# Kernel optimization log

Hardware: AMD Instinct MI355X
Metric: run time of the kernel (lower is better)

## Reference

```python
import jax, jax.numpy as jnp
import numpy as np

DIM = 1024
NH = 16
HD = DIM // NH  # 64
NT = max(1, int(NH * 0.25))  # 4 time heads
NS = NH - NT                 # 12 space heads
SCALE = HD ** (-0.5)


def setup_inputs() -> dict:
    key = jax.random.key(0)
    ks = jax.random.split(key, 8)
    B, T = 2, 2048
    init = 0.02
    return {
        "x": jax.random.normal(ks[0], (B, T, DIM), dtype=jnp.float32),
        # weights stored as (in, out); torch Linear y = x @ W.T is equivalent
        "Wqt": jax.random.normal(ks[1], (DIM, NT * HD), dtype=jnp.float32) * init,
        "Wkt": jax.random.normal(ks[2], (DIM, NT * HD), dtype=jnp.float32) * init,
        "Wqs": jax.random.normal(ks[3], (DIM, NS * HD), dtype=jnp.float32) * init,
        "Wks": jax.random.normal(ks[4], (DIM, NS * HD), dtype=jnp.float32) * init,
        "Wv": jax.random.normal(ks[5], (DIM, DIM), dtype=jnp.float32) * init,
        "Wout": jax.random.normal(ks[6], (DIM, DIM), dtype=jnp.float32) * init,
        "bout": jnp.zeros((DIM,), dtype=jnp.float32),
        "w_sigma": jnp.zeros((1,), dtype=jnp.float32),
    }


def reference(x, Wqt, Wkt, Wqs, Wks, Wv, Wout, bout, w_sigma):
    B, T, D = x.shape
    Qt = (x @ Wqt).reshape(B, T, NT, HD)
    Kt = (x @ Wkt).reshape(B, T, NT, HD)
    Qs = (x @ Wqs).reshape(B, T, NS, HD)
    Ks = (x @ Wks).reshape(B, T, NS, HD)
    st = jnp.einsum('bthd,bshd->bths', Qt, Kt)  # [B,T,NT,T]
    ss = jnp.einsum('bthd,bshd->bths', Qs, Ks)  # [B,T,NS,T]
    sig = jax.nn.sigmoid(w_sigma)  # shape (1,), broadcasts
    score = jnp.concatenate([-sig * st, ss], axis=2) * SCALE  # [B,T,NH,T]
    attn = jax.nn.softmax(score, axis=-1)
    V = (x @ Wv).reshape(B, T, NH, HD)
    ctx = jnp.einsum('bths,bshd->bthd', attn, V).reshape(B, T, D)
    return ctx @ Wout + bout
```

## Files before the change

### kernel.cpp

```cpp
#include <hip/hip_runtime.h>
#include <hip/hip_bf16.h>

typedef __bf16 bf16_t;
typedef __bf16 bf16x4 __attribute__((ext_vector_type(4)));
typedef __bf16 bf16x8 __attribute__((ext_vector_type(8)));
typedef float  f32x4  __attribute__((ext_vector_type(4)));

#define DIM     1024
#define NHEAD   16
#define HDIM    64
#define NTIME   4
#define TSEQ    2048
#define NBATCH  2
#define SCALE_F 0.125f
#define LOG2E   1.4426950408889634f

#define GLL(gp, lp) __builtin_amdgcn_global_load_lds( \
    (const __attribute__((address_space(1))) unsigned int*)(const void*)(gp), \
    (__attribute__((address_space(3))) unsigned int*)(void*)(lp), 16, 0, 0)

#define OFF_WQKVT 0UL
#define OFF_WOUTT (OFF_WQKVT + 3072UL*1024UL*2UL)
#define OFF_Q     (OFF_WOUTT + 1024UL*1024UL*2UL)
#define OFF_K     (OFF_Q  + 2UL*16UL*2048UL*64UL*2UL)
#define OFF_VT    (OFF_K  + 2UL*16UL*2048UL*64UL*2UL)
#define OFF_CTX   (OFF_VT + 2UL*16UL*2048UL*64UL*2UL)

__global__ void prep_all(const float* __restrict__ x,
                         const float* __restrict__ Wqt, const float* __restrict__ Wkt,
                         const float* __restrict__ Wqs, const float* __restrict__ Wks,
                         const float* __restrict__ Wv,  const float* __restrict__ Wout,
                         bf16_t* __restrict__ Xb, bf16_t* __restrict__ WqkvT,
                         bf16_t* __restrict__ WoutT) {
    __shared__ float T[64][65];
    const int bid = blockIdx.x;
    if (bid < 2048) {
        int i = bid * 256 + threadIdx.x;
        const float4* s = (const float4*)(x + (size_t)i * 8);
        float4 a = s[0], b2 = s[1];
        bf16x8 v;
        v[0] = (bf16_t)a.x;  v[1] = (bf16_t)a.y;  v[2] = (bf16_t)a.z;  v[3] = (bf16_t)a.w;
        v[4] = (bf16_t)b2.x; v[5] = (bf16_t)b2.y; v[6] = (bf16_t)b2.z; v[7] = (bf16_t)b2.w;
        *(bf16x8*)(Xb + (size_t)i * 8) = v;
        return;
    }
    const int tc = threadIdx.x & 63, tr = threadIdx.x >> 6;
    if (bid < 2816) {
        const int l = bid - 2048;
        const int n0 = (l % 48) * 64;
        const int k0 = (l / 48) * 64;
        const int region = n0 >> 10;
        const int cc = n0 & 1023;
        const int h = cc >> 6;
        const float* src; int ncols, col0;
        if (region == 2) { src = Wv; ncols = 1024; col0 = cc; }
        else if (h < NTIME) { src = (region == 0) ? Wqt : Wkt; ncols = NTIME * HDIM; col0 = h * HDIM; }
        else                { src = (region == 0) ? Wqs : Wks; ncols = (NHEAD - NTIME) * HDIM; col0 = (h - NTIME) * HDIM; }
#pragma unroll
        for (int i = 0; i < 16; ++i) {
            int kl = tr * 16 + i;
            T[kl][tc] = src[(size_t)(k0 + kl) * ncols + col0 + tc];
        }
        __syncthreads();
#pragma unroll
        for (int i = 0; i < 16; ++i) {
            int nl = tr * 16 + i;
            WqkvT[(size_t)(n0 + nl) * 1024 + k0 + tc] = (bf16_t)T[tc][nl];
        }
    } else {
        const int l = bid - 2816;
        const int n0 = (l % 16) * 64;
        const int k0 = (l / 16) * 64;
#pragma unroll
        for (int i = 0; i < 16; ++i) {
            int kl = tr * 16 + i;
            T[kl][tc] = Wout[(size_t)(k0 + kl) * 1024 + n0 + tc];
        }
        __syncthreads();
#pragma unroll
        for (int i = 0; i < 16; ++i) {
            int nl = tr * 16 + i;
            WoutT[(size_t)(n0 + nl) * 1024 + k0 + tc] = (bf16_t)T[tc][nl];
        }
    }
}

template<int MODE, int NB>
__global__ __launch_bounds__(256)
void gemm_bf16(const bf16_t* __restrict__ Ab, const bf16_t* __restrict__ Bt,
               bf16_t* __restrict__ Qb, bf16_t* __restrict__ Kb, bf16_t* __restrict__ Vt,
               float* __restrict__ Cout, const float* __restrict__ bias)
{
    __shared__ __align__(16) bf16_t As[3][128][32];
    __shared__ __align__(16) bf16_t Bs[3][128][32];

    constexpr int NXC = NB / 8;
    const int xcd = blockIdx.x & 7;
    const int r   = blockIdx.x >> 3;
    const int m0 = (r / NXC) * 128;
    const int n0 = (xcd * NXC + r % NXC) * 128;

    const int tid  = threadIdx.x;
    const int lane = tid & 63;
    const int wave = tid >> 6;
    const int wm = (wave >> 1) * 64, wn = (wave & 1) * 64;
    const int g = lane >> 4, lr = lane & 15;

    f32x4 acc[4][4];
#pragma unroll
    for (int i = 0; i < 4; ++i)
#pragma unroll
        for (int j = 0; j < 4; ++j) acc[i][j] = f32x4{0.f, 0.f, 0.f, 0.f};

    auto stage = [&](int k0, int buf) {
#pragma unroll
        for (int c = 0; c < 2; ++c) {
            int idx  = tid + c * 256;
            int row  = idx >> 2;
            int csrc = (idx & 3) ^ ((row >> 1) & 3);
            GLL(Ab + (size_t)(m0 + row) * 1024 + k0 + csrc * 8,
                (char*)&As[buf][0][0] + (c * 256 + wave * 64) * 16);
            GLL(Bt + (size_t)(n0 + row) * 1024 + k0 + csrc * 8,
                (char*)&Bs[buf][0][0] + (c * 256 + wave * 64) * 16);
        }
    };

    stage(0, 0);
    stage(32, 1);

    for (int t = 0; t < 32; ++t) {
        if (t < 31) asm volatile("s_waitcnt vmcnt(4)" ::: "memory");
        else        asm volatile("s_waitcnt vmcnt(0)" ::: "memory");
        __builtin_amdgcn_s_barrier();
        __builtin_amdgcn_sched_barrier(0);
        if (t + 2 < 32) stage((t + 2) * 32, (t + 2) % 3);

        const int buf = t % 3;
        const char* Ac = (const char*)&As[buf][0][0];
        const char* Bc = (const char*)&Bs[buf][0][0];
        bf16x8 afr[4], bfr[4];
#pragma unroll
        for (int f = 0; f < 4; ++f) {
            int ra = wm + f * 16 + lr;
            afr[f] = *(const bf16x8*)(Ac + ra * 64 + ((g ^ ((ra >> 1) & 3)) << 4));
            int rb = wn + f * 16 + lr;
            bfr[f] = *(const bf16x8*)(Bc + rb * 64 + ((g ^ ((rb >> 1) & 3)) << 4));
        }
        __builtin_amdgcn_s_setprio(1);
#pragma unroll
        for (int fm = 0; fm < 4; ++fm)
#pragma unroll
            for (int fn = 0; fn < 4; ++fn)
                acc[fm][fn] = __builtin_amdgcn_mfma_f32_16x16x32_bf16(bfr[fn], afr[fm], acc[fm][fn], 0, 0, 0);
        __builtin_amdgcn_s_setprio(0);
    }

    const int region = n0 >> 10;
#pragma unroll
    for (int fm = 0; fm < 4; ++fm) {
        const int m = m0 + wm + fm * 16 + lr;
        const int b = m >> 11, t = m & 2047;
        const int ts = (t & ~31) | (((t >> 2) & 3) << 3) | (((t >> 4) & 1) << 2) | (t & 3);
#pragma unroll
        for (int fn = 0; fn < 4; ++fn) {
            const int nb = n0 + wn + fn * 16 + g * 4;
            if constexpr (MODE == 1) {
                float4 bb = *(const float4*)(bias + nb);
                float4 v;
                v.x = acc[fm][fn][0] + bb.x;
                v.y = acc[fm][fn][1] + bb.y;
                v.z = acc[fm][fn][2] + bb.z;
                v.w = acc[fm][fn][3] + bb.w;
                *(float4*)(Cout + (size_t)m * DIM + nb) = v;
            } else {
                const int cc = nb & 1023;
                const int h = cc >> 6, d0 = cc & 63;
                const size_t bh = (size_t)(b * NHEAD + h);
                if (region == 2) {
#pragma unroll
                    for (int r2 = 0; r2 < 4; ++r2)
                        Vt[(bh * HDIM + d0 + r2) * TSEQ + ts] = (bf16_t)acc[fm][fn][r2];
                } else {
                    bf16x4 w;
#pragma unroll
                    for (int r2 = 0; r2 < 4; ++r2) w[r2] = (bf16_t)acc[fm][fn][r2];
                    bf16_t* dst = (region == 0) ? Qb : Kb;
                    *(bf16x4*)(dst + (bh * TSEQ + t) * HDIM + d0) = w;
                }
            }
        }
    }
}

__global__ __launch_bounds__(256, 2)
void attn_kernel(const bf16_t* __restrict__ Qb, const bf16_t* __restrict__ Kb,
                 const bf16_t* __restrict__ Vt, bf16_t* __restrict__ ctx,
                 const float* __restrict__ w_sigma)
{
    __shared__ __align__(16) bf16_t Ktile[4][64][64];
    __shared__ __align__(16) bf16_t Vtile[4][64][64];

    const int l    = ((blockIdx.x & 7) << 6) + (blockIdx.x >> 3);
    const int qc   = l & 15;
    const int bh   = l >> 4;
    const int h    = bh & 15;
    const int b    = bh >> 4;
    const int tid  = threadIdx.x;
    const int lane = tid & 63;
    const int wave = tid >> 6;
    const int g = lane >> 4, lr = lane & 15;
    const int q0 = qc * 128 + wave * 32;

    const float sig = 1.f / (1.f + __expf(-w_sigma[0]));
    const float fl2 = ((h < NTIME) ? (-sig * SCALE_F) : SCALE_F) * LOG2E;

    const bf16_t* Qp = Qb + (size_t)bh * TSEQ * HDIM;
    const bf16_t* Kp = Kb + (size_t)bh * TSEQ * HDIM;
    const bf16_t* Vp = Vt + (size_t)bh * HDIM * TSEQ;

    bf16x8 qa0 = *(const bf16x8*)(Qp + (size_t)(q0 + lr) * HDIM + g * 8);
    bf16x8 qa1 = *(const bf16x8*)(Qp + (size_t)(q0 + lr) * HDIM + 32 + g * 8);
    bf16x8 qb0 = *(const bf16x8*)(Qp + (size_t)(q0 + 16 + lr) * HDIM + g * 8);
    bf16x8 qb1 = *(const bf16x8*)(Qp + (size_t)(q0 + 16 + lr) * HDIM + 32 + g * 8);
#pragma unroll
    for (int e = 0; e < 8; ++e) {
        qa0[e] = (bf16_t)((float)qa0[e] * fl2);
        qa1[e] = (bf16_t)((float)qa1[e] * fl2);
        qb0[e] = (bf16_t)((float)qb0[e] * fl2);
        qb1[e] = (bf16_t)((float)qb1[e] * fl2);
    }

    f32x4 oA[4], oB[4];
#pragma unroll
    for (int n = 0; n < 4; ++n) { oA[n] = f32x4{0.f,0.f,0.f,0.f}; oB[n] = f32x4{0.f,0.f,0.f,0.f}; }
    float lpA = 0.f, lpB = 0.f;

    const int trow = tid >> 3;
    const int tcg  = tid & 7;

    auto stage = [&](int s0, int buf) {
#pragma unroll
        for (int j = 0; j < 2; ++j) {
            int kr = j * 32 + trow;
            GLL(Kp + (size_t)(s0 + kr) * HDIM + ((tcg ^ (kr & 7)) << 3),
                (char*)&Ktile[buf][0][0] + (j * 256 + wave * 64) * 16);
            int vr = j * 32 + trow;
            GLL(Vp + (size_t)vr * TSEQ + s0 + ((tcg ^ (vr & 7)) << 3),
                (char*)&Vtile[buf][0][0] + (j * 256 + wave * 64) * 16);
        }
    };

    auto compute = [&](const char* Kt, const char* Vc) {
        bf16x4 wA[4], wB[4];
        __builtin_amdgcn_s_setprio(1);
#pragma unroll
        for (int st = 0; st < 4; ++st) {
            const int srow = st * 16 + lr;
            const int rs7 = lr & 7;
            bf16x8 kb0 = *(const bf16x8*)(Kt + srow * 128 + ((g ^ rs7) << 4));
            bf16x8 kb1 = *(const bf16x8*)(Kt + srow * 128 + (((4 + g) ^ rs7) << 4));
            f32x4 zA = f32x4{0.f,0.f,0.f,0.f}, zB = f32x4{0.f,0.f,0.f,0.f};
            zA = __builtin_amdgcn_mfma_f32_16x16x32_bf16(kb0, qa0, zA, 0, 0, 0);
            zA = __builtin_amdgcn_mfma_f32_16x16x32_bf16(kb1, qa1, zA, 0, 0, 0);
            zB = __builtin_amdgcn_mfma_f32_16x16x32_bf16(kb0, qb0, zB, 0, 0, 0);
            zB = __builtin_amdgcn_mfma_f32_16x16x32_bf16(kb1, qb1, zB, 0, 0, 0);
            float a0 = __builtin_amdgcn_exp2f(zA[0]);
            float a1 = __builtin_amdgcn_exp2f(zA[1]);
            float a2 = __builtin_amdgcn_exp2f(zA[2]);
            float a3 = __builtin_amdgcn_exp2f(zA[3]);
            float b0 = __builtin_amdgcn_exp2f(zB[0]);
            float b1 = __builtin_amdgcn_exp2f(zB[1]);
            float b2 = __builtin_amdgcn_exp2f(zB[2]);
            float b3 = __builtin_amdgcn_exp2f(zB[3]);
            wA[st][0] = (bf16_t)a0; wA[st][1] = (bf16_t)a1; wA[st][2] = (bf16_t)a2; wA[st][3] = (bf16_t)a3;
            wB[st][0] = (bf16_t)b0; wB[st][1] = (bf16_t)b1; wB[st][2] = (bf16_t)b2; wB[st][3] = (bf16_t)b3;
            lpA += (a0 + a1) + (a2 + a3);
            lpB += (b0 + b1) + (b2 + b3);
        }
        __builtin_amdgcn_s_setprio(0);

        __builtin_amdgcn_s_setprio(1);
#pragma unroll
        for (int kc = 0; kc < 2; ++kc) {
            bf16x8 paA, paB;
#pragma unroll
            for (int e = 0; e < 4; ++e) {
                paA[e]     = wA[kc * 2][e];
                paA[e + 4] = wA[kc * 2 + 1][e];
                paB[e]     = wB[kc * 2][e];
                paB[e + 4] = wB[kc * 2 + 1][e];
            }
#pragma unroll
            for (int n = 0; n < 4; ++n) {
                const int row = n * 16 + lr;
                bf16x8 vb = *(const bf16x8*)(Vc + row * 128 + (((kc * 4 + g) ^ (row & 7)) << 4));
                oA[n] = __builtin_amdgcn_mfma_f32_16x16x32_bf16(vb, paA, oA[n], 0, 0, 0);
                oB[n] = __builtin_amdgcn_mfma_f32_16x16x32_bf16(vb, paB, oB[n], 0, 0, 0);
            }
        }
        __builtin_amdgcn_s_setprio(0);
    };

    stage(0, 0);
    stage(64, 1);

    for (int step = 0; step < 32; ++step) {
        if (step + 2 < 32) stage((step + 2) * 64, (step + 2) & 3);
        if (step < 30)       asm volatile("s_waitcnt vmcnt(8)" ::: "memory");
        else if (step == 30) asm volatile("s_waitcnt vmcnt(4)" ::: "memory");
        else                 asm volatile("s_waitcnt vmcnt(0)" ::: "memory");
        __builtin_amdgcn_s_barrier();
        __builtin_amdgcn_sched_barrier(0);
        const int buf = step & 3;
        compute((const char*)&Ktile[buf][0][0], (const char*)&Vtile[buf][0][0]);
    }

    float lfA = lpA, lfB = lpB;
    lfA += __shfl_xor(lfA, 16, 64);
    lfA += __shfl_xor(lfA, 32, 64);
    lfB += __shfl_xor(lfB, 16, 64);
    lfB += __shfl_xor(lfB, 32, 64);
    float liA = 1.f / lfA, liB = 1.f / lfB;

    const int tA = q0 + lr, tB = q0 + 16 + lr;
#pragma unroll
    for (int n = 0; n < 4; ++n) {
        bf16x4 wA, wB;
#pragma unroll
        for (int r = 0; r < 4; ++r) {
            wA[r] = (bf16_t)(oA[n][r] * liA);
            wB[r] = (bf16_t)(oB[n][r] * liB);
        }
        *(bf16x4*)(ctx + ((size_t)(b * TSEQ + tA)) * DIM + h * HDIM + n * 16 + g * 4) = wA;
        *(bf16x4*)(ctx + ((size_t)(b * TSEQ + tB)) * DIM + h * HDIM + n * 16 + g * 4) = wB;
    }
}

extern "C" void kernel_launch(void* const* d_in, const int* in_sizes, int n_in,
                              void* d_out, int out_size, void* d_ws, size_t ws_size,
                              hipStream_t stream) {
    const float* x    = (const float*)d_in[0];
    const float* Wqt  = (const float*)d_in[1];
    const float* Wkt  = (const float*)d_in[2];
    const float* Wqs  = (const float*)d_in[3];
    const float* Wks  = (const float*)d_in[4];
    const float* Wv   = (const float*)d_in[5];
    const float* Wout = (const float*)d_in[6];
    const float* bout = (const float*)d_in[7];
    const float* wsig = (const float*)d_in[8];
    (void)in_sizes; (void)n_in; (void)out_size; (void)ws_size;

    char* ws = (char*)d_ws;
    bf16_t* WqkvT = (bf16_t*)(ws + OFF_WQKVT);
    bf16_t* WoutT = (bf16_t*)(ws + OFF_WOUTT);
    bf16_t* Qb    = (bf16_t*)(ws + OFF_Q);
    bf16_t* Kb    = (bf16_t*)(ws + OFF_K);
    bf16_t* Vt    = (bf16_t*)(ws + OFF_VT);
    bf16_t* ctx   = (bf16_t*)(ws + OFF_CTX);
    bf16_t* Xb    = ctx;
    float*  out   = (float*)d_out;

    prep_all<<<3072, 256, 0, stream>>>(x, Wqt, Wkt, Wqs, Wks, Wv, Wout, Xb, WqkvT, WoutT);

    gemm_bf16<0, 24><<<768, 256, 0, stream>>>(Xb, WqkvT, Qb, Kb, Vt, nullptr, nullptr);

    attn_kernel<<<512, 256, 0, stream>>>(Qb, Kb, Vt, ctx, wsig);

    gemm_bf16<1, 8><<<256, 256, 0, stream>>>(ctx, WoutT, nullptr, nullptr, nullptr, out, bout);
}
```

Measured before the change: 111.6 us.

## Split attention over key halves with separate normalize pass and narrower output GEMM tiles

```diff
diff --git a/kernel.cpp b/kernel.cpp
--- a/kernel.cpp
+++ b/kernel.cpp
@@ -85,32 +85,32 @@
     }
 }
 
-template<int MODE, int NB>
+template<int MODE, int NB, int FN>
 __global__ __launch_bounds__(256)
 void gemm_bf16(const bf16_t* __restrict__ Ab, const bf16_t* __restrict__ Bt,
                bf16_t* __restrict__ Qb, bf16_t* __restrict__ Kb, bf16_t* __restrict__ Vt,
                float* __restrict__ Cout, const float* __restrict__ bias)
 {
     __shared__ __align__(16) bf16_t As[3][128][32];
-    __shared__ __align__(16) bf16_t Bs[3][128][32];
+    __shared__ __align__(16) bf16_t Bs[3][FN * 32][32];
 
     constexpr int NXC = NB / 8;
     const int xcd = blockIdx.x & 7;
     const int r   = blockIdx.x >> 3;
     const int m0 = (r / NXC) * 128;
-    const int n0 = (xcd * NXC + r % NXC) * 128;
+    const int n0 = (xcd * NXC + r % NXC) * (FN * 32);
 
     const int tid  = threadIdx.x;
     const int lane = tid & 63;
     const int wave = tid >> 6;
-    const int wm = (wave >> 1) * 64, wn = (wave & 1) * 64;
+    const int wm = (wave >> 1) * 64, wn = (wave & 1) * (FN * 16);
     const int g = lane >> 4, lr = lane & 15;
 
-    f32x4 acc[4][4];
+    f32x4 acc[4][FN];
 #pragma unroll
     for (int i = 0; i < 4; ++i)
 #pragma unroll
-        for (int j = 0; j < 4; ++j) acc[i][j] = f32x4{0.f, 0.f, 0.f, 0.f};
+        for (int j = 0; j < FN; ++j) acc[i][j] = f32x4{0.f, 0.f, 0.f, 0.f};
 
     auto stage = [&](int k0, int buf) {
 #pragma unroll
@@ -120,8 +120,9 @@
             int csrc = (idx & 3) ^ ((row >> 1) & 3);
             GLL(Ab + (size_t)(m0 + row) * 1024 + k0 + csrc * 8,
                 (char*)&As[buf][0][0] + (c * 256 + wave * 64) * 16);
-            GLL(Bt + (size_t)(n0 + row) * 1024 + k0 + csrc * 8,
-                (char*)&Bs[buf][0][0] + (c * 256 + wave * 64) * 16);
+            if (c < FN / 2)
+                GLL(Bt + (size_t)(n0 + row) * 1024 + k0 + csrc * 8,
+                    (char*)&Bs[buf][0][0] + (c * 256 + wave * 64) * 16);
         }
     };
 
@@ -129,8 +130,12 @@
     stage(32, 1);
 
     for (int t = 0; t < 32; ++t) {
-        if (t < 31) asm volatile("s_waitcnt vmcnt(4)" ::: "memory");
-        else        asm volatile("s_waitcnt vmcnt(0)" ::: "memory");
+        if (t < 31) {
+            if constexpr (FN == 4) asm volatile("s_waitcnt vmcnt(4)" ::: "memory");
+            else                   asm volatile("s_waitcnt vmcnt(3)" ::: "memory");
+        } else {
+            asm volatile("s_waitcnt vmcnt(0)" ::: "memory");
+        }
         __builtin_amdgcn_s_barrier();
         __builtin_amdgcn_sched_barrier(0);
         if (t + 2 < 32) stage((t + 2) * 32, (t + 2) % 3);
@@ -138,11 +143,14 @@
         const int buf = t % 3;
         const char* Ac = (const char*)&As[buf][0][0];
         const char* Bc = (const char*)&Bs[buf][0][0];
-        bf16x8 afr[4], bfr[4];
+        bf16x8 afr[4], bfr[FN];
 #pragma unroll
         for (int f = 0; f < 4; ++f) {
             int ra = wm + f * 16 + lr;
             afr[f] = *(const bf16x8*)(Ac + ra * 64 + ((g ^ ((ra >> 1) & 3)) << 4));
+        }
+#pragma unroll
+        for (int f = 0; f < FN; ++f) {
             int rb = wn + f * 16 + lr;
             bfr[f] = *(const bf16x8*)(Bc + rb * 64 + ((g ^ ((rb >> 1) & 3)) << 4));
         }
@@ -150,7 +158,7 @@
 #pragma unroll
         for (int fm = 0; fm < 4; ++fm)
 #pragma unroll
-            for (int fn = 0; fn < 4; ++fn)
+            for (int fn = 0; fn < FN; ++fn)
                 acc[fm][fn] = __builtin_amdgcn_mfma_f32_16x16x32_bf16(bfr[fn], afr[fm], acc[fm][fn], 0, 0, 0);
         __builtin_amdgcn_s_setprio(0);
     }
@@ -162,7 +170,7 @@
         const int b = m >> 11, t = m & 2047;
         const int ts = (t & ~31) | (((t >> 2) & 3) << 3) | (((t >> 4) & 1) << 2) | (t & 3);
 #pragma unroll
-        for (int fn = 0; fn < 4; ++fn) {
+        for (int fn = 0; fn < FN; ++fn) {
             const int nb = n0 + wn + fn * 16 + g * 4;
             if constexpr (MODE == 1) {
                 float4 bb = *(const float4*)(bias + nb);
@@ -192,24 +200,27 @@
     }
 }
 
-__global__ __launch_bounds__(256, 2)
+__global__ __launch_bounds__(256, 4)
 void attn_kernel(const bf16_t* __restrict__ Qb, const bf16_t* __restrict__ Kb,
-                 const bf16_t* __restrict__ Vt, bf16_t* __restrict__ ctx,
-                 const float* __restrict__ w_sigma)
+                 const bf16_t* __restrict__ Vt, bf16_t* __restrict__ ctxp,
+                 float* __restrict__ outp, float* __restrict__ l0,
+                 float* __restrict__ l1, const float* __restrict__ w_sigma)
 {
-    __shared__ __align__(16) bf16_t Ktile[4][64][64];
-    __shared__ __align__(16) bf16_t Vtile[4][64][64];
-
-    const int l    = ((blockIdx.x & 7) << 6) + (blockIdx.x >> 3);
-    const int qc   = l & 15;
-    const int bh   = l >> 4;
-    const int h    = bh & 15;
-    const int b    = bh >> 4;
-    const int tid  = threadIdx.x;
-    const int lane = tid & 63;
-    const int wave = tid >> 6;
+    __shared__ __align__(16) bf16_t Ktile[4][32][64];
+    __shared__ __align__(16) bf16_t Vtile[4][64][32];
+
+    const int l     = ((blockIdx.x & 7) << 7) + (blockIdx.x >> 3);
+    const int qc    = l & 15;
+    const int shalf = (l >> 4) & 1;
+    const int bh    = l >> 5;
+    const int h     = bh & 15;
+    const int b     = bh >> 4;
+    const int tid   = threadIdx.x;
+    const int lane  = tid & 63;
+    const int wave  = tid >> 6;
     const int g = lane >> 4, lr = lane & 15;
     const int q0 = qc * 128 + wave * 32;
+    const int sbase = shalf * 1024;
 
     const float sig = 1.f / (1.f + __expf(-w_sigma[0]));
     const float fl2 = ((h < NTIME) ? (-sig * SCALE_F) : SCALE_F) * LOG2E;
@@ -235,26 +246,21 @@
     for (int n = 0; n < 4; ++n) { oA[n] = f32x4{0.f,0.f,0.f,0.f}; oB[n] = f32x4{0.f,0.f,0.f,0.f}; }
     float lpA = 0.f, lpB = 0.f;
 
-    const int trow = tid >> 3;
-    const int tcg  = tid & 7;
+    const int rowK = tid >> 3, cgK = tid & 7;
+    const int rowV = tid >> 2, cgV = tid & 3;
 
     auto stage = [&](int s0, int buf) {
-#pragma unroll
-        for (int j = 0; j < 2; ++j) {
-            int kr = j * 32 + trow;
-            GLL(Kp + (size_t)(s0 + kr) * HDIM + ((tcg ^ (kr & 7)) << 3),
-                (char*)&Ktile[buf][0][0] + (j * 256 + wave * 64) * 16);
-            int vr = j * 32 + trow;
-            GLL(Vp + (size_t)vr * TSEQ + s0 + ((tcg ^ (vr & 7)) << 3),
-                (char*)&Vtile[buf][0][0] + (j * 256 + wave * 64) * 16);
-        }
+        GLL(Kp + (size_t)(s0 + rowK) * HDIM + ((cgK ^ (rowK & 7)) << 3),
+            (char*)&Ktile[buf][0][0] + wave * 1024);
+        GLL(Vp + (size_t)rowV * TSEQ + s0 + ((cgV ^ ((rowV >> 1) & 3)) << 3),
+            (char*)&Vtile[buf][0][0] + wave * 1024);
     };
 
     auto compute = [&](const char* Kt, const char* Vc) {
-        bf16x4 wA[4], wB[4];
+        bf16x4 wA[2], wB[2];
         __builtin_amdgcn_s_setprio(1);
 #pragma unroll
-        for (int st = 0; st < 4; ++st) {
+        for (int st = 0; st < 2; ++st) {
             const int srow = st * 16 + lr;
             const int rs7 = lr & 7;
             bf16x8 kb0 = *(const bf16x8*)(Kt + srow * 128 + ((g ^ rs7) << 4));
@@ -277,37 +283,29 @@
             lpA += (a0 + a1) + (a2 + a3);
             lpB += (b0 + b1) + (b2 + b3);
         }
-        __builtin_amdgcn_s_setprio(0);
-
-        __builtin_amdgcn_s_setprio(1);
-#pragma unroll
-        for (int kc = 0; kc < 2; ++kc) {
-            bf16x8 paA, paB;
-#pragma unroll
-            for (int e = 0; e < 4; ++e) {
-                paA[e]     = wA[kc * 2][e];
-                paA[e + 4] = wA[kc * 2 + 1][e];
-                paB[e]     = wB[kc * 2][e];
-                paB[e + 4] = wB[kc * 2 + 1][e];
-            }
-#pragma unroll
-            for (int n = 0; n < 4; ++n) {
-                const int row = n * 16 + lr;
-                bf16x8 vb = *(const bf16x8*)(Vc + row * 128 + (((kc * 4 + g) ^ (row & 7)) << 4));
-                oA[n] = __builtin_amdgcn_mfma_f32_16x16x32_bf16(vb, paA, oA[n], 0, 0, 0);
-                oB[n] = __builtin_amdgcn_mfma_f32_16x16x32_bf16(vb, paB, oB[n], 0, 0, 0);
-            }
+        bf16x8 paA, paB;
+#pragma unroll
+        for (int e = 0; e < 4; ++e) {
+            paA[e] = wA[0][e]; paA[e + 4] = wA[1][e];
+            paB[e] = wB[0][e]; paB[e + 4] = wB[1][e];
+        }
+#pragma unroll
+        for (int n = 0; n < 4; ++n) {
+            const int row = n * 16 + lr;
+            bf16x8 vb = *(const bf16x8*)(Vc + row * 64 + ((g ^ ((row >> 1) & 3)) << 4));
+            oA[n] = __builtin_amdgcn_mfma_f32_16x16x32_bf16(vb, paA, oA[n], 0, 0, 0);
+            oB[n] = __builtin_amdgcn_mfma_f32_16x16x32_bf16(vb, paB, oB[n], 0, 0, 0);
         }
         __builtin_amdgcn_s_setprio(0);
     };
 
-    stage(0, 0);
-    stage(64, 1);
+    stage(sbase, 0);
+    stage(sbase + 32, 1);
 
     for (int step = 0; step < 32; ++step) {
-        if (step + 2 < 32) stage((step + 2) * 64, (step + 2) & 3);
-        if (step < 30)       asm volatile("s_waitcnt vmcnt(8)" ::: "memory");
-        else if (step == 30) asm volatile("s_waitcnt vmcnt(4)" ::: "memory");
+        if (step + 2 < 32) stage(sbase + (step + 2) * 32, (step + 2) & 3);
+        if (step < 30)       asm volatile("s_waitcnt vmcnt(4)" ::: "memory");
+        else if (step == 30) asm volatile("s_waitcnt vmcnt(2)" ::: "memory");
         else                 asm volatile("s_waitcnt vmcnt(0)" ::: "memory");
         __builtin_amdgcn_s_barrier();
         __builtin_amdgcn_sched_barrier(0);
@@ -320,20 +318,52 @@
     lfA += __shfl_xor(lfA, 32, 64);
     lfB += __shfl_xor(lfB, 16, 64);
     lfB += __shfl_xor(lfB, 32, 64);
-    float liA = 1.f / lfA, liB = 1.f / lfB;
 
     const int tA = q0 + lr, tB = q0 + 16 + lr;
-#pragma unroll
-    for (int n = 0; n < 4; ++n) {
-        bf16x4 wA, wB;
-#pragma unroll
-        for (int r = 0; r < 4; ++r) {
-            wA[r] = (bf16_t)(oA[n][r] * liA);
-            wB[r] = (bf16_t)(oB[n][r] * liB);
-        }
-        *(bf16x4*)(ctx + ((size_t)(b * TSEQ + tA)) * DIM + h * HDIM + n * 16 + g * 4) = wA;
-        *(bf16x4*)(ctx + ((size_t)(b * TSEQ + tB)) * DIM + h * HDIM + n * 16 + g * 4) = wB;
-    }
+    if (shalf == 0) {
+#pragma unroll
+        for (int n = 0; n < 4; ++n) {
+            *(f32x4*)(outp + ((size_t)(b * TSEQ + tA)) * DIM + h * HDIM + n * 16 + g * 4) = oA[n];
+            *(f32x4*)(outp + ((size_t)(b * TSEQ + tB)) * DIM + h * HDIM + n * 16 + g * 4) = oB[n];
+        }
+    } else {
+#pragma unroll
+        for (int n = 0; n < 4; ++n) {
+            bf16x4 wA2, wB2;
+#pragma unroll
+            for (int r = 0; r < 4; ++r) { wA2[r] = (bf16_t)oA[n][r]; wB2[r] = (bf16_t)oB[n][r]; }
+            *(bf16x4*)(ctxp + ((size_t)(b * TSEQ + tA)) * DIM + h * HDIM + n * 16 + g * 4) = wA2;
+            *(bf16x4*)(ctxp + ((size_t)(b * TSEQ + tB)) * DIM + h * HDIM + n * 16 + g * 4) = wB2;
+        }
+    }
+    if (g == 0) {
+        float* lb = shalf ? l1 : l0;
+        lb[bh * TSEQ + q0 + lr]      = lfA;
+        lb[bh * TSEQ + q0 + 16 + lr] = lfB;
+    }
+}
+
+__global__ void normalize_ctx(const float* __restrict__ outp, const float* __restrict__ l0,
+                              const float* __restrict__ l1, bf16_t* __restrict__ ctx)
+{
+    const int idx = blockIdx.x * 256 + threadIdx.x;
+    const int d8 = idx & 7;
+    const int hh = (idx >> 3) & 15;
+    const int tt = (idx >> 7) & 2047;
+    const int bb = idx >> 18;
+    const int bh = bb * 16 + hh;
+    const float li = 1.f / (l0[bh * TSEQ + tt] + l1[bh * TSEQ + tt]);
+    const size_t base = ((size_t)(bb * TSEQ + tt)) * DIM + hh * HDIM + d8 * 8;
+    const f32x4* pf = (const f32x4*)(outp + base);
+    f32x4 a = pf[0], c = pf[1];
+    bf16x8 p1 = *(const bf16x8*)(ctx + base);
+    bf16x8 w;
+#pragma unroll
+    for (int j = 0; j < 4; ++j) {
+        w[j]     = (bf16_t)((a[j] + (float)p1[j])     * li);
+        w[j + 4] = (bf16_t)((c[j] + (float)p1[j + 4]) * li);
+    }
+    *(bf16x8*)(ctx + base) = w;
 }
 
 extern "C" void kernel_launch(void* const* d_in, const int* in_sizes, int n_in,
@@ -358,13 +388,17 @@
     bf16_t* Vt    = (bf16_t*)(ws + OFF_VT);
     bf16_t* ctx   = (bf16_t*)(ws + OFF_CTX);
     bf16_t* Xb    = ctx;
-    float*  out   = (float*)d_out;
+    float* l0 = (float*)(ws + OFF_WQKVT);
+    float* l1 = l0 + 32 * TSEQ;
+    float* out = (float*)d_out;
 
     prep_all<<<3072, 256, 0, stream>>>(x, Wqt, Wkt, Wqs, Wks, Wv, Wout, Xb, WqkvT, WoutT);
 
-    gemm_bf16<0, 24><<<768, 256, 0, stream>>>(Xb, WqkvT, Qb, Kb, Vt, nullptr, nullptr);
-
-    attn_kernel<<<512, 256, 0, stream>>>(Qb, Kb, Vt, ctx, wsig);
-
-    gemm_bf16<1, 8><<<256, 256, 0, stream>>>(ctx, WoutT, nullptr, nullptr, nullptr, out, bout);
+    gemm_bf16<0, 24, 4><<<768, 256, 0, stream>>>(Xb, WqkvT, Qb, Kb, Vt, nullptr, nullptr);
+
+    attn_kernel<<<1024, 256, 0, stream>>>(Qb, Kb, Vt, ctx, out, l0, l1, wsig);
+
+    normalize_ctx<<<2048, 256, 0, stream>>>(out, l0, l1, ctx);
+
+    gemm_bf16<1, 16, 2><<<512, 256, 0, stream>>>(ctx, WoutT, nullptr, nullptr, nullptr, out, bout);
 }
```

Result: slower. 117.8 us (+5.5%).
